# Kernel optimization log

Measured on AMD Instinct MI355X. Metric: run time of the kernel, lower is better.

Reference implementation:

```python
import jax, jax.numpy as jnp
import numpy as np

D = 16      # chem_dims
K = 16      # hard-coded k in Atom_embedding
N = 81920   # query points
M = 20000   # atoms
EPS = 1e-5  # BatchNorm eps


def _knn_idx(x, y, x_batch, y_batch, k, chunk=1024):
    """Block-diagonal kNN: indices of k nearest atoms in y for each point in x,
    restricted to matching batch ids (mirrors pykeops diagonal_ranges)."""
    n = x.shape[0]
    nch = n // chunk
    yb = y_batch[None, :]

    def f(args):
        xc, xbc = args                                            # [chunk,3], [chunk]
        d = jnp.sum((xc[:, None, :] - y[None, :, :]) ** 2, -1)    # [chunk, M]
        d = jnp.where(xbc[:, None] == yb, d, jnp.inf)
        _, idx = jax.lax.top_k(-d, k)                             # k smallest dists
        return idx

    idx = jax.lax.map(f, (x.reshape(nch, chunk, 3), x_batch.reshape(nch, chunk)))
    return idx.reshape(n, k)


def _bn_eval(h, gamma, beta, mean, var):
    # eval-mode BatchNorm1d over last dim
    return (h - mean) * (gamma * jax.lax.rsqrt(var + EPS)) + beta


def setup_inputs() -> dict:
    key = jax.random.key(0)
    ks = jax.random.split(key, 12)
    inp = {
        "x": jax.random.uniform(ks[0], (N, 3), jnp.float32) * 10.0,
        "y": jax.random.uniform(ks[1], (M, 3), jnp.float32) * 10.0,
        "y_atomtypes": jax.random.normal(ks[2], (M, D), jnp.float32),
        "x_batch": jnp.zeros((N,), jnp.int32),
        "y_batch": jnp.zeros((M,), jnp.int32),
        "W1": jax.random.normal(ks[3], (D + 1, D), jnp.float32) * 0.1,
        "b1": jnp.zeros((D,), jnp.float32),
        "W2": jax.random.normal(ks[4], (D, D), jnp.float32) * 0.1,
        "b2": jnp.zeros((D,), jnp.float32),
        "W3": jax.random.normal(ks[5], (2 * D, D), jnp.float32) * 0.1,
        "b3": jnp.zeros((D,), jnp.float32),
        "bn1_g": jnp.ones((D,), jnp.float32),
        "bn1_b": jnp.zeros((D,), jnp.float32),
        "bn1_m": jax.random.normal(ks[6], (D,), jnp.float32) * 0.1,
        "bn1_v": jnp.ones((D,), jnp.float32),
        "bn2_g": jnp.ones((D,), jnp.float32),
        "bn2_b": jnp.zeros((D,), jnp.float32),
        "bn2_m": jax.random.normal(ks[7], (D,), jnp.float32) * 0.1,
        "bn2_v": jnp.ones((D,), jnp.float32),
    }
    return inp


def reference(x, y, y_atomtypes, x_batch, y_batch,
              W1, b1, W2, b2, W3, b3,
              bn1_g, bn1_b, bn1_m, bn1_v,
              bn2_g, bn2_b, bn2_m, bn2_v):
    idx = _knn_idx(x, y, x_batch, y_batch, K)            # [N, K] int32
    yk = y[idx]                                          # [N, K, 3]
    dists = jnp.sum((x[:, None, :] - yk) ** 2, -1)       # [N, K]
    feat = jnp.concatenate(
        [y_atomtypes[idx], (1.0 / dists)[..., None]], -1)  # [N, K, D+1]
    # dropout in eval mode == identity
    h = feat @ W1 + b1                                   # conv1
    h = _bn_eval(jax.nn.leaky_relu(h, 0.2), bn1_g, bn1_b, bn1_m, bn1_v)
    fx1 = jnp.sum(h, axis=1)                             # [N, D]
    h2 = h @ W2 + b2                                     # conv2
    h2 = _bn_eval(jax.nn.leaky_relu(h2, 0.2), bn2_g, bn2_b, bn2_m, bn2_v)
    fx2 = jnp.sum(h2, axis=1)                            # [N, D]
    out = jnp.concatenate([fx1, fx2], -1) @ W3 + b3      # conv3 -> [N, D]
    return out
```

## Files before the change

kernel.cpp:

```cpp
#include <hip/hip_runtime.h>

#define N_PTS 81920
#define M_PTS 20000
#define NC 13
#define NCELLS 2197
#define CELLW 0.7692307692f
#define INVCELL 1.3f
#define BIGF 3.0e38f
#define CAP_STAGE 312
#define PPC 16
#define WPB 4
#define MAX_TASKS 7320

__device__ __forceinline__ int clampi(int v, int lo, int hi) {
  return v < lo ? lo : (v > hi ? hi : v);
}
__device__ __forceinline__ int cell_coord(float p) {
  return clampi((int)(p * INVCELL), 0, NC - 1);
}
__device__ __forceinline__ float floorpack(float d) {
  return __uint_as_float(__float_as_uint(d) & 0xFFFF8000u);
}


__global__ void hist_both_kernel(const float* __restrict__ y, const float* __restrict__ x,
                                 int* __restrict__ ycnt, int* __restrict__ xcnt) {
  int i = blockIdx.x * blockDim.x + threadIdx.x;
  if (i < M_PTS) {
    int c = (cell_coord(y[3*i+2])*NC + cell_coord(y[3*i+1]))*NC + cell_coord(y[3*i]);
    atomicAdd(&ycnt[c], 1);
  } else {
    int j = i - M_PTS;
    if (j < N_PTS) {
      int c = (cell_coord(x[3*j+2])*NC + cell_coord(x[3*j+1]))*NC + cell_coord(x[3*j]);
      atomicAdd(&xcnt[c], 1);
    }
  }
}

__global__ void scan2_kernel(const int* __restrict__ ycnt, int* __restrict__ ystart, int* __restrict__ ycur,
                             const int* __restrict__ xcnt, int* __restrict__ xstart, int* __restrict__ xcur) {
  const int* cnt = (blockIdx.x == 0) ? ycnt : xcnt;
  int* start     = (blockIdx.x == 0) ? ystart : xstart;
  int* cursor    = (blockIdx.x == 0) ? ycur : xcur;
  __shared__ int tmp[1024];
  int tid = threadIdx.x;
  int chunk = (NCELLS + 1023) >> 10;
  int base = tid * chunk;
  int sum = 0;
  for (int k = 0; k < chunk; ++k) {
    int j = base + k;
    if (j < NCELLS) sum += cnt[j];
  }
  tmp[tid] = sum;
  __syncthreads();
  for (int off = 1; off < 1024; off <<= 1) {
    int v = (tid >= off) ? tmp[tid - off] : 0;
    __syncthreads();
    tmp[tid] += v;
    __syncthreads();
  }
  int run = tmp[tid] - sum;
  for (int k = 0; k < chunk; ++k) {
    int j = base + k;
    if (j < NCELLS) { start[j] = run; cursor[j] = run; run += cnt[j]; }
  }
  if (tid == 1023) start[NCELLS] = tmp[1023];
}

__global__ void scatter_both_kernel(const float* __restrict__ y, const float* __restrict__ x,
                                    int* __restrict__ ycur, int* __restrict__ xcur,
                                    float4* __restrict__ ys4, int* __restrict__ xorder,
                                    float4* __restrict__ xs4) {
  int i = blockIdx.x * blockDim.x + threadIdx.x;
  if (i < M_PTS) {
    float px = y[3*i], py = y[3*i+1], pz = y[3*i+2];
    int c = (cell_coord(pz)*NC + cell_coord(py))*NC + cell_coord(px);
    int pos = atomicAdd(&ycur[c], 1);
    ys4[pos] = make_float4(px, py, pz, __int_as_float(i));
  } else {
    int j = i - M_PTS;
    if (j < N_PTS) {
      float px = x[3*j], py = x[3*j+1], pz = x[3*j+2];
      int c = (cell_coord(pz)*NC + cell_coord(py))*NC + cell_coord(px);
      int pos = atomicAdd(&xcur[c], 1);
      xorder[pos] = j;
      if (xs4) xs4[pos] = make_float4(px, py, pz, __int_as_float(j));
    }
  }
}

__global__ void build_tasks_kernel(const int* __restrict__ xstart,
                                   int* __restrict__ tasks, int* __restrict__ ntasks) {
  int c = blockIdx.x * blockDim.x + threadIdx.x;
  if (c >= NCELLS) return;
  int cnt = xstart[c+1] - xstart[c];
  int nch = (cnt + PPC - 1) / PPC;
  if (nch > 0) {
    int pos = atomicAdd(ntasks, nch);
    for (int k = 0; k < nch; ++k) tasks[pos + k] = (k << 12) | c;
  }
}

__global__ void sortcell_kernel(float4* __restrict__ ys4, const int* __restrict__ ystart) {
  int c = blockIdx.x * blockDim.x + threadIdx.x;
  if (c >= NCELLS) return;
  int r0 = ystart[c], r1 = ystart[c+1];
  for (int i = r0 + 1; i < r1; ++i) {
    float4 v = ys4[i];
    int key = __float_as_int(v.w);
    int j = i - 1;
    while (j >= r0 && __float_as_int(ys4[j].w) > key) { ys4[j+1] = ys4[j]; --j; }
    ys4[j+1] = v;
  }
}

__device__ __forceinline__ void bitonic_sort16(float (&d)[16]) {
  #define CE(a,b) { float lo=fminf(d[a],d[b]); float hi=fmaxf(d[a],d[b]); d[a]=lo; d[b]=hi; }
  CE(0,8) CE(1,9) CE(2,10) CE(3,11) CE(4,12) CE(5,13) CE(6,14) CE(7,15)
  CE(0,4) CE(1,5) CE(2,6) CE(3,7) CE(8,12) CE(9,13) CE(10,14) CE(11,15)
  CE(0,2) CE(1,3) CE(4,6) CE(5,7) CE(8,10) CE(9,11) CE(12,14) CE(13,15)
  CE(0,1) CE(2,3) CE(4,5) CE(6,7) CE(8,9) CE(10,11) CE(12,13) CE(14,15)
  #undef CE
}

__device__ __forceinline__ void ins16(float (&s)[16], float k) {
  #pragma unroll
  for (int j = 15; j >= 1; --j) s[j] = fminf(fmaxf(s[j-1], k), s[j]);
  s[0] = fminf(s[0], k);
}

__global__ void __launch_bounds__(256) knn_cell_kernel(
    const float4* __restrict__ xs4,
    const float4* __restrict__ ys4, const int* __restrict__ ystart,
    const int* __restrict__ xstart,
    const int* __restrict__ tasks, const int* __restrict__ ntasks,
    unsigned short* __restrict__ pi)
{
  __shared__ float4 cand_all[WPB][CAP_STAGE];
  int wid = threadIdx.x >> 6;
  int tid = threadIdx.x & 63;
  int ti = blockIdx.x * WPB + wid;
  if (ti >= ntasks[0]) return;
  int task = tasks[ti];
  int c = task & 4095, chunk = task >> 12;
  int cbeg = xstart[c];
  int cend = xstart[c+1];
  int pbeg = cbeg + chunk*PPC;
  int pend = min(cend, pbeg + PPC);

  float4* cand = cand_all[wid];

  int ccx = c % NC, ccy = (c / NC) % NC, ccz = c / (NC*NC);
  int x0 = ccx-1 < 0 ? 0 : ccx-1, x1 = ccx+1 > NC-1 ? NC-1 : ccx+1;
  int y0 = ccy-1 < 0 ? 0 : ccy-1, y1 = ccy+1 > NC-1 ? NC-1 : ccy+1;
  int z0 = ccz-1 < 0 ? 0 : ccz-1, z1 = ccz+1 > NC-1 ? NC-1 : ccz+1;

  int off = 0, nst = 0; bool ovf = false;
  for (int gz = z0; gz <= z1; ++gz) {
    for (int gy = y0; gy <= y1; ++gy) {
      int rowbase = (gz*NC + gy)*NC;
      int r0 = ystart[rowbase + x0];
      int r1 = ystart[rowbase + x1 + 1];
      int len = r1 - r0;
      if (!ovf && off + len <= CAP_STAGE) {
        for (int k = tid; k < len; k += 64) cand[off + k] = ys4[r0 + k];
        off += len; ++nst;
      } else ovf = true;
    }
  }
  int L = off;
  asm volatile("s_waitcnt vmcnt(0) lgkmcnt(0)" ::: "memory");

  int g = tid >> 2, sub = tid & 3;
  int pidx = pbeg + g;
  bool active = pidx < pend;
  int gid = active ? pidx : (pend - 1);
  float4 xq = xs4[gid];
  float xpx = xq.x, xpy = xq.y, xpz = xq.z;

  float s[16];
  #pragma unroll
  for (int j = 0; j < 16; ++j) s[j] = BIGF;

  auto packkey = [&](float4 q) -> float {
    float dx = xpx - q.x, dy = xpy - q.y, dz = xpz - q.z;
    float d = fmaf(dx, dx, fmaf(dy, dy, dz*dz));
    unsigned kb = (__float_as_uint(d) & 0xFFFF8000u) | (__float_as_uint(q.w) & 0x7FFFu);
    return __uint_as_float(kb);
  };

  auto merged16 = [&](float (&u)[16]) {
    float cb[16];
    #pragma unroll
    for (int i = 0; i < 16; ++i) cb[i] = fminf(s[i], __shfl_xor(s[15-i], 1));
    bitonic_sort16(cb);
    #pragma unroll
    for (int i = 0; i < 16; ++i) u[i] = fminf(cb[i], __shfl_xor(cb[15-i], 2));
    bitonic_sort16(u);
  };

  {
    int i = sub;
    for (; i + 4 < L; i += 8) {
      float4 q0 = cand[i], q1 = cand[i+4];
      float k0 = packkey(q0), k1 = packkey(q1);
      ins16(s, k0); ins16(s, k1);
    }
    for (; i < L; i += 4) ins16(s, packkey(cand[i]));
  }

  auto scan_row_g = [&](int xa, int xb, int rowbase) {
    int r0 = ystart[rowbase + xa];
    int r1 = ystart[rowbase + xb + 1];
    int i = r0 + sub;
    for (; i + 4 < r1; i += 8) {
      float4 q0 = ys4[i], q1 = ys4[i+4];
      float k0 = packkey(q0), k1 = packkey(q1);
      ins16(s, k0); ins16(s, k1);
    }
    for (; i < r1; i += 4) ins16(s, packkey(ys4[i]));
  };

  if (ovf) {
    int cnt2 = 0;
    for (int gz = z0; gz <= z1; ++gz)
      for (int gy = y0; gy <= y1; ++gy) {
        if (cnt2 >= nst) scan_row_g(x0, x1, (gz*NC + gy)*NC);
        ++cnt2;
      }
  }

  float u[16];
  merged16(u);
  float s15m = u[15];
  int R = 1;
  while (true) {
    float b = BIGF;
    if (ccx - R >= 0)    b = fminf(b, xpx - (float)(ccx-R)*CELLW);
    if (ccx + R <= NC-2) b = fminf(b, (float)(ccx+R+1)*CELLW - xpx);
    if (ccy - R >= 0)    b = fminf(b, xpy - (float)(ccy-R)*CELLW);
    if (ccy + R <= NC-2) b = fminf(b, (float)(ccy+R+1)*CELLW - xpy);
    if (ccz - R >= 0)    b = fminf(b, xpz - (float)(ccz-R)*CELLW);
    if (ccz + R <= NC-2) b = fminf(b, (float)(ccz+R+1)*CELLW - xpz);
    b = fmaxf(b - 1e-4f, 0.0f);
    if (s15m <= floorpack(b*b) || R >= NC) break;
    ++R;
    int z0r = ccz-R < 0 ? 0 : ccz-R, z1r = ccz+R > NC-1 ? NC-1 : ccz+R;
    int y0r = ccy-R < 0 ? 0 : ccy-R, y1r = ccy+R > NC-1 ? NC-1 : ccy+R;
    int x0r = ccx-R < 0 ? 0 : ccx-R, x1r = ccx+R > NC-1 ? NC-1 : ccx+R;
    for (int gz = z0r; gz <= z1r; ++gz) {
      int dzz = gz - ccz; if (dzz < 0) dzz = -dzz;
      float gapz = (gz > ccz) ? ((float)gz*CELLW - xpz)
                 : ((gz < ccz) ? (xpz - (float)(gz+1)*CELLW) : 0.0f);
      gapz = fmaxf(gapz - 1e-4f, 0.0f);
      float gz2 = gapz * gapz;
      for (int gy = y0r; gy <= y1r; ++gy) {
        int dyy = gy - ccy; if (dyy < 0) dyy = -dyy;
        float gapy = (gy > ccy) ? ((float)gy*CELLW - xpy)
                   : ((gy < ccy) ? (xpy - (float)(gy+1)*CELLW) : 0.0f);
        gapy = fmaxf(gapy - 1e-4f, 0.0f);
        float rowd2 = fmaf(gapy, gapy, gz2);
        if (floorpack(rowd2) >= s15m) continue;
        int rowbase = (gz*NC + gy)*NC;
        if (dzz == R || dyy == R) {
          scan_row_g(x0r, x1r, rowbase);
        } else {
          if (ccx - R >= 0) {
            float gapx = fmaxf(xpx - (float)(ccx-R+1)*CELLW - 1e-4f, 0.0f);
            if (floorpack(fmaf(gapx, gapx, rowd2)) < s15m)
              scan_row_g(ccx-R, ccx-R, rowbase);
          }
          if (ccx + R <= NC-1) {
            float gapx = fmaxf((float)(ccx+R)*CELLW - xpx - 1e-4f, 0.0f);
            if (floorpack(fmaf(gapx, gapx, rowd2)) < s15m)
              scan_row_g(ccx+R, ccx+R, rowbase);
          }
        }
      }
    }
    merged16(u);
    s15m = u[15];
  }

  if (active) {
    float v0 = u[sub*4+0], v1 = u[sub*4+1], v2 = u[sub*4+2], v3 = u[sub*4+3];
    unsigned wlo = (__float_as_uint(v0) & 0x7FFFu) | ((__float_as_uint(v1) & 0x7FFFu) << 16);
    unsigned whi = (__float_as_uint(v2) & 0x7FFFu) | ((__float_as_uint(v3) & 0x7FFFu) << 16);
    uint2 W; W.x = wlo; W.y = whi;
    ((uint2*)pi)[gid*4 + sub] = W;
  }
}

template<int CTRL>
__device__ __forceinline__ float ror_add(float v) {
  int r = __builtin_amdgcn_update_dpp(0, __float_as_int(v), CTRL, 0xF, 0xF, true);
  return v + __int_as_float(r);
}
__device__ __forceinline__ float red16(float v) {
  v = ror_add<0x121>(v);
  v = ror_add<0x122>(v);
  v = ror_add<0x124>(v);
  v = ror_add<0x128>(v);
  return v;
}

__global__ void __launch_bounds__(256) mlp_kernel(
    const float* __restrict__ yat, const float4* __restrict__ xs4, const float* __restrict__ y,
    const float* __restrict__ W1, const float* __restrict__ b1,
    const float* __restrict__ W2, const float* __restrict__ b2,
    const float* __restrict__ W3, const float* __restrict__ b3,
    const float* __restrict__ g1, const float* __restrict__ be1,
    const float* __restrict__ m1, const float* __restrict__ v1,
    const float* __restrict__ g2, const float* __restrict__ be2,
    const float* __restrict__ m2, const float* __restrict__ v2,
    const unsigned short* __restrict__ pi, float* __restrict__ out)
{
  int t = threadIdx.x;
  int o = t & 15;
  int gid = (blockIdx.x * 256 + t) >> 4;
  float4 xq = xs4[gid];
  int p = __float_as_int(xq.w);

  int id = (int)pi[gid*16 + o];
  float dx = xq.x - y[3*id], dy = xq.y - y[3*id+1], dz = xq.z - y[3*id+2];
  float dist = fmaf(dx, dx, fmaf(dy, dy, dz*dz));
  float invd = 1.0f / dist;

  const float4* a4 = (const float4*)(yat + ((size_t)id << 4));
  float4 q0 = a4[0], q1 = a4[1], q2 = a4[2], q3 = a4[3];
  float a[16];
  a[0]=q0.x; a[1]=q0.y; a[2]=q0.z; a[3]=q0.w;
  a[4]=q1.x; a[5]=q1.y; a[6]=q1.z; a[7]=q1.w;
  a[8]=q2.x; a[9]=q2.y; a[10]=q2.z; a[11]=q2.w;
  a[12]=q3.x; a[13]=q3.y; a[14]=q3.z; a[15]=q3.w;

  float h[16];
  #pragma unroll
  for (int oo = 0; oo < 16; ++oo) {
    float acc = fmaf(invd, W1[256 + oo], b1[oo]);
    #pragma unroll
    for (int i = 0; i < 16; ++i) acc = fmaf(a[i], W1[i*16 + oo], acc);
    acc = fmaxf(acc, 0.2f * acc);
    float S = g1[oo] * rsqrtf(v1[oo] + 1e-5f);
    h[oo] = fmaf(acc - m1[oo], S, be1[oo]);
  }

  float f2[16];
  #pragma unroll
  for (int oo = 0; oo < 16; ++oo) {
    float acc = b2[oo];
    #pragma unroll
    for (int i = 0; i < 16; ++i) acc = fmaf(h[i], W2[i*16 + oo], acc);
    acc = fmaxf(acc, 0.2f * acc);
    float S = g2[oo] * rsqrtf(v2[oo] + 1e-5f);
    f2[oo] = fmaf(acc - m2[oo], S, be2[oo]);
  }

  float acc = b3[o];
  #pragma unroll
  for (int i = 0; i < 16; ++i) acc = fmaf(red16(h[i]),  W3[i*16 + o], acc);
  #pragma unroll
  for (int i = 0; i < 16; ++i) acc = fmaf(red16(f2[i]), W3[(16 + i)*16 + o], acc);

  out[(size_t)p*16 + o] = acc;
}

__device__ __forceinline__ void stage_weights(float* lds, int t,
    const float* W1, const float* b1, const float* W2, const float* b2,
    const float* W3, const float* b3,
    const float* g1, const float* be1, const float* m1, const float* v1,
    const float* g2, const float* be2, const float* m2, const float* v2)
{
  for (int k = t; k < 272; k += 256) { int i = k >> 4, o = k & 15; lds[o*20 + i] = W1[k]; }
  for (int k = t; k < 256; k += 256) { int i = k >> 4, o = k & 15; lds[320 + o*16 + i] = W2[k]; }
  for (int k = t; k < 512; k += 256) { int i = k >> 4, o = k & 15; lds[576 + o*32 + i] = W3[k]; }
  if (t < 16) {
    lds[1088 + t] = b1[t];
    lds[1104 + t] = b2[t];
    lds[1120 + t] = b3[t];
    float s1 = g1[t] * rsqrtf(v1[t] + 1e-5f);
    lds[1136 + t] = s1;
    lds[1152 + t] = be1[t] - m1[t]*s1;
    float s2 = g2[t] * rsqrtf(v2[t] + 1e-5f);
    lds[1168 + t] = s2;
    lds[1184 + t] = be2[t] - m2[t]*s2;
  }
}

__device__ __forceinline__ void topk_insert(float (&s)[16], int (&si)[16], float d, int qi) {
  #pragma unroll
  for (int j = 15; j >= 1; --j) {
    bool c1 = d < s[j-1];
    bool c2 = d < s[j];
    float ns = c1 ? s[j-1] : (c2 ? d : s[j]);
    int  ni = c1 ? si[j-1] : (c2 ? qi : si[j]);
    s[j] = ns; si[j] = ni;
  }
  if (d < s[0]) { si[0] = qi; s[0] = d; }
}

__device__ __forceinline__ void mlp_and_store(const float* lds, const float2* spill, int t,
    const float* __restrict__ yat, float* __restrict__ out, int p)
{
  const float* W1t = lds;
  const float* W2t = lds + 320;
  const float* W3t = lds + 576;
  const float* sb1 = lds + 1088;
  const float* sb2 = lds + 1104;
  const float* sb3 = lds + 1120;
  const float* S1 = lds + 1136;
  const float* T1 = lds + 1152;
  const float* S2 = lds + 1168;
  const float* T2 = lds + 1184;

  float fx1[16], fx2[16];
  #pragma unroll
  for (int o = 0; o < 16; ++o) { fx1[o] = 0.0f; fx2[o] = 0.0f; }

  #pragma unroll 1
  for (int j = 0; j < 16; ++j) {
    float2 sv = spill[j*256 + t];
    float invd = 1.0f / sv.x;
    int id = __float_as_int(sv.y);
    const float4* a4 = (const float4*)(yat + ((size_t)id << 4));
    float4 q0 = a4[0], q1 = a4[1], q2 = a4[2], q3 = a4[3];
    float a[16];
    a[0]=q0.x; a[1]=q0.y; a[2]=q0.z; a[3]=q0.w;
    a[4]=q1.x; a[5]=q1.y; a[6]=q1.z; a[7]=q1.w;
    a[8]=q2.x; a[9]=q2.y; a[10]=q2.z; a[11]=q2.w;
    a[12]=q3.x; a[13]=q3.y; a[14]=q3.z; a[15]=q3.w;
    float h[16];
    #pragma unroll
    for (int o = 0; o < 16; ++o) {
      float acc = fmaf(invd, W1t[o*20 + 16], sb1[o]);
      #pragma unroll
      for (int i = 0; i < 16; ++i) acc = fmaf(a[i], W1t[o*20 + i], acc);
      acc = fmaxf(acc, 0.2f * acc);
      float hv = fmaf(acc, S1[o], T1[o]);
      h[o] = hv;
      fx1[o] += hv;
    }
    #pragma unroll
    for (int o = 0; o < 16; ++o) {
      float acc = sb2[o];
      #pragma unroll
      for (int i = 0; i < 16; ++i) acc = fmaf(h[i], W2t[o*16 + i], acc);
      acc = fmaxf(acc, 0.2f * acc);
      fx2[o] += fmaf(acc, S2[o], T2[o]);
    }
  }

  float res[16];
  #pragma unroll
  for (int o = 0; o < 16; ++o) {
    float acc = sb3[o];
    #pragma unroll
    for (int i = 0; i < 16; ++i) acc = fmaf(fx1[i], W3t[o*32 + i], acc);
    #pragma unroll
    for (int i = 0; i < 16; ++i) acc = fmaf(fx2[i], W3t[o*32 + 16 + i], acc);
    res[o] = acc;
  }
  float* op = out + ((size_t)p << 4);
  float4 r;
  r.x=res[0]; r.y=res[1]; r.z=res[2]; r.w=res[3];   ((float4*)op)[0] = r;
  r.x=res[4]; r.y=res[5]; r.z=res[6]; r.w=res[7];   ((float4*)op)[1] = r;
  r.x=res[8]; r.y=res[9]; r.z=res[10]; r.w=res[11]; ((float4*)op)[2] = r;
  r.x=res[12]; r.y=res[13]; r.z=res[14]; r.w=res[15];((float4*)op)[3] = r;
}

__global__ void __launch_bounds__(256) knn_mlp_fused_kernel(
    const float* __restrict__ x, const float* __restrict__ yat,
    const float* __restrict__ W1, const float* __restrict__ b1,
    const float* __restrict__ W2, const float* __restrict__ b2,
    const float* __restrict__ W3, const float* __restrict__ b3,
    const float* __restrict__ g1, const float* __restrict__ be1,
    const float* __restrict__ m1, const float* __restrict__ v1,
    const float* __restrict__ g2, const float* __restrict__ be2,
    const float* __restrict__ m2, const float* __restrict__ v2,
    const float4* __restrict__ ys4, const int* __restrict__ ystart,
    const int* __restrict__ xorder, float* __restrict__ out)
{
  __shared__ float lds[1200];
  __shared__ float2 spill[4096];
  int t = threadIdx.x;
  stage_weights(lds, t, W1,b1,W2,b2,W3,b3, g1,be1,m1,v1, g2,be2,m2,v2);
  __syncthreads();

  int gid = blockIdx.x * 256 + t;
  int p = xorder[gid];
  float xpx = x[3*p], xpy = x[3*p+1], xpz = x[3*p+2];
  int cx = cell_coord(xpx), cy = cell_coord(xpy), cz = cell_coord(xpz);

  float s[16]; int si[16];
  #pragma unroll
  for (int j = 0; j < 16; ++j) { s[j] = BIGF; si[j] = 0; }

  auto scan_row = [&](int gz, int gy, int xa, int xb) {
    int rowbase = (gz*NC + gy)*NC;
    int r0 = ystart[rowbase + xa];
    int r1 = ystart[rowbase + xb + 1];
    for (int i = r0; i < r1; ++i) {
      float4 q = ys4[i];
      float dx = xpx - q.x, dy = xpy - q.y, dz = xpz - q.z;
      float d = fmaf(dx, dx, fmaf(dy, dy, dz*dz));
      if (d < s[15]) topk_insert(s, si, d, __float_as_int(q.w));
    }
  };

  {
    int z0 = cz-1 < 0 ? 0 : cz-1, z1 = cz+1 > NC-1 ? NC-1 : cz+1;
    int y0 = cy-1 < 0 ? 0 : cy-1, y1 = cy+1 > NC-1 ? NC-1 : cy+1;
    int x0 = cx-1 < 0 ? 0 : cx-1, x1 = cx+1 > NC-1 ? NC-1 : cx+1;
    for (int gz = z0; gz <= z1; ++gz)
      for (int gy = y0; gy <= y1; ++gy)
        scan_row(gz, gy, x0, x1);
  }

  int R = 1;
  while (true) {
    float b = BIGF;
    if (cx - R >= 0)    b = fminf(b, xpx - (float)(cx-R)*CELLW);
    if (cx + R <= NC-2) b = fminf(b, (float)(cx+R+1)*CELLW - xpx);
    if (cy - R >= 0)    b = fminf(b, xpy - (float)(cy-R)*CELLW);
    if (cy + R <= NC-2) b = fminf(b, (float)(cy+R+1)*CELLW - xpy);
    if (cz - R >= 0)    b = fminf(b, xpz - (float)(cz-R)*CELLW);
    if (cz + R <= NC-2) b = fminf(b, (float)(cz+R+1)*CELLW - xpz);
    b = fmaxf(b - 1e-4f, 0.0f);
    if (s[15] <= b*b || R >= NC) break;
    ++R;
    int z0 = cz-R < 0 ? 0 : cz-R, z1 = cz+R > NC-1 ? NC-1 : cz+R;
    int y0 = cy-R < 0 ? 0 : cy-R, y1 = cy+R > NC-1 ? NC-1 : cy+R;
    int x0 = cx-R < 0 ? 0 : cx-R, x1 = cx+R > NC-1 ? NC-1 : cx+R;
    for (int gz = z0; gz <= z1; ++gz) {
      int dzz = gz - cz; if (dzz < 0) dzz = -dzz;
      for (int gy = y0; gy <= y1; ++gy) {
        int dyy = gy - cy; if (dyy < 0) dyy = -dyy;
        if (dzz == R || dyy == R) {
          scan_row(gz, gy, x0, x1);
        } else {
          if (cx - R >= 0)    scan_row(gz, gy, cx-R, cx-R);
          if (cx + R <= NC-1) scan_row(gz, gy, cx+R, cx+R);
        }
      }
    }
  }

  #pragma unroll
  for (int j = 0; j < 16; ++j) spill[j*256 + t] = make_float2(s[j], __int_as_float(si[j]));
  mlp_and_store(lds, spill, t, yat, out, p);
}

__global__ void __launch_bounds__(256) brute_kernel(
    const float* __restrict__ x, const float* __restrict__ y, const float* __restrict__ yat,
    const float* __restrict__ W1, const float* __restrict__ b1,
    const float* __restrict__ W2, const float* __restrict__ b2,
    const float* __restrict__ W3, const float* __restrict__ b3,
    const float* __restrict__ g1, const float* __restrict__ be1,
    const float* __restrict__ m1, const float* __restrict__ v1,
    const float* __restrict__ g2, const float* __restrict__ be2,
    const float* __restrict__ m2, const float* __restrict__ v2,
    float* __restrict__ out)
{
  __shared__ float lds[1200];
  __shared__ float2 spill[4096];
  __shared__ float4 ybuf[1024];
  int t = threadIdx.x;
  stage_weights(lds, t, W1,b1,W2,b2,W3,b3, g1,be1,m1,v1, g2,be2,m2,v2);

  int gid = blockIdx.x * 256 + t;
  float xpx = x[3*gid], xpy = x[3*gid+1], xpz = x[3*gid+2];
  float s[16]; int si[16];
  #pragma unroll
  for (int j = 0; j < 16; ++j) { s[j] = BIGF; si[j] = 0; }

  for (int base = 0; base < M_PTS; base += 1024) {
    int nload = M_PTS - base; if (nload > 1024) nload = 1024;
    __syncthreads();
    for (int k = t; k < nload; k += 256) {
      int i = base + k;
      ybuf[k] = make_float4(y[3*i], y[3*i+1], y[3*i+2], __int_as_float(i));
    }
    __syncthreads();
    for (int i2 = 0; i2 < nload; ++i2) {
      float4 q = ybuf[i2];
      float dx = xpx - q.x, dy = xpy - q.y, dz = xpz - q.z;
      float d = fmaf(dx, dx, fmaf(dy, dy, dz*dz));
      if (d < s[15]) topk_insert(s, si, d, __float_as_int(q.w));
    }
  }

  #pragma unroll
  for (int j = 0; j < 16; ++j) spill[j*256 + t] = make_float2(s[j], __int_as_float(si[j]));
  mlp_and_store(lds, spill, t, yat, out, gid);
}

extern "C" void kernel_launch(void* const* d_in, const int* in_sizes, int n_in,
                              void* d_out, int out_size, void* d_ws, size_t ws_size,
                              hipStream_t stream) {
  const float* x   = (const float*)d_in[0];
  const float* y   = (const float*)d_in[1];
  const float* yat = (const float*)d_in[2];
  const float* W1  = (const float*)d_in[5];
  const float* b1  = (const float*)d_in[6];
  const float* W2  = (const float*)d_in[7];
  const float* b2  = (const float*)d_in[8];
  const float* W3  = (const float*)d_in[9];
  const float* b3  = (const float*)d_in[10];
  const float* g1  = (const float*)d_in[11];
  const float* be1 = (const float*)d_in[12];
  const float* m1  = (const float*)d_in[13];
  const float* v1  = (const float*)d_in[14];
  const float* g2  = (const float*)d_in[15];
  const float* be2 = (const float*)d_in[16];
  const float* m2  = (const float*)d_in[17];
  const float* v2  = (const float*)d_in[18];
  float* out = (float*)d_out;

  const size_t WS_SPLIT = 4661936;
  const size_t WS_FUSED = 700480;

  if (ws_size >= WS_SPLIT) {
    char* ws = (char*)d_ws;
    float4* ys4 = (float4*)(ws);
    float4* xs4 = (float4*)(ws + 320000);
    int* xorder = (int*)(ws + 1630720);
    unsigned short* pi = (unsigned short*)(ws + 1958400);
    int* ycnt   = (int*)(ws + 4579840);
    int* xcnt   = (int*)(ws + 4588640);
    int* ystart = (int*)(ws + 4597440);
    int* ycur   = (int*)(ws + 4606240);
    int* xstart = (int*)(ws + 4615040);
    int* xcur   = (int*)(ws + 4623840);
    int* ntasks = (int*)(ws + 4632640);
    int* tasks  = (int*)(ws + 4632656);

    hipMemsetAsync(ws + 4579840, 0, 17600, stream);
    hipMemsetAsync(ws + 4632640, 0, 16, stream);
    int grid_mn = (M_PTS + N_PTS + 255) / 256;
    hist_both_kernel<<<grid_mn, 256, 0, stream>>>(y, x, ycnt, xcnt);
    scan2_kernel<<<2, 1024, 0, stream>>>(ycnt, ystart, ycur, xcnt, xstart, xcur);
    scatter_both_kernel<<<grid_mn, 256, 0, stream>>>(y, x, ycur, xcur, ys4, xorder, xs4);
    build_tasks_kernel<<<(NCELLS+255)/256, 256, 0, stream>>>(xstart, tasks, ntasks);
    knn_cell_kernel<<<MAX_TASKS/WPB, 256, 0, stream>>>(xs4, ys4, ystart, xstart,
        tasks, ntasks, pi);
    mlp_kernel<<<(N_PTS*16)/256, 256, 0, stream>>>(yat, xs4, y, W1,b1,W2,b2,W3,b3,
        g1,be1,m1,v1, g2,be2,m2,v2, pi, out);
  } else if (ws_size >= WS_FUSED) {
    char* ws = (char*)d_ws;
    float4* ys4 = (float4*)(ws);
    int* xorder = (int*)(ws + 320000);
    int* ycnt   = (int*)(ws + 647680);
    int* xcnt   = (int*)(ws + 656480);
    int* ystart = (int*)(ws + 665280);
    int* ycur   = (int*)(ws + 674080);
    int* xstart = (int*)(ws + 682880);
    int* xcur   = (int*)(ws + 691680);

    hipMemsetAsync(ws + 647680, 0, 17588, stream);
    int grid_mn = (M_PTS + N_PTS + 255) / 256;
    hist_both_kernel<<<grid_mn, 256, 0, stream>>>(y, x, ycnt, xcnt);
    scan2_kernel<<<2, 1024, 0, stream>>>(ycnt, ystart, ycur, xcnt, xstart, xcur);
    scatter_both_kernel<<<grid_mn, 256, 0, stream>>>(y, x, ycur, xcur, ys4, xorder, nullptr);
    sortcell_kernel<<<(NCELLS+255)/256, 256, 0, stream>>>(ys4, ystart);
    knn_mlp_fused_kernel<<<N_PTS/256, 256, 0, stream>>>(x, yat, W1,b1,W2,b2,W3,b3,
        g1,be1,m1,v1, g2,be2,m2,v2, ys4, ystart, xorder, out);
  } else {
    brute_kernel<<<N_PTS/256, 256, 0, stream>>>(x, y, yat, W1,b1,W2,b2,W3,b3,
        g1,be1,m1,v1, g2,be2,m2,v2, out);
  }
}
```

Before: 122.3 us.

## Refine grid to 14^3 cells, fold task building into scan, pad atom coords

The spatial grid goes from 13^3 to 14^3 cells, so each cell holds fewer atoms and kNN candidate scanning shrinks, with the staging capacity and max task count adjusted to match. Task-list construction moves into the second block of the scan kernel as a deterministic prefix sum, which removes the separate build_tasks launch and its atomics along with one memset. The scatter kernel also writes a float4-padded copy of the atom coordinates so the MLP kernel can load each neighbor's position in one vector read instead of three scalar reads. The costs are a larger workspace requirement, a serial per-thread task write loop in the scan, and a smaller staging capacity that could overflow for dense cells.

```diff
diff --git a/kernel.cpp b/kernel.cpp
--- a/kernel.cpp
+++ b/kernel.cpp
@@ -2,15 +2,15 @@
 
 #define N_PTS 81920
 #define M_PTS 20000
-#define NC 13
-#define NCELLS 2197
-#define CELLW 0.7692307692f
-#define INVCELL 1.3f
+#define NC 14
+#define NCELLS 2744
+#define CELLW 0.7142857143f
+#define INVCELL 1.4f
 #define BIGF 3.0e38f
-#define CAP_STAGE 312
+#define CAP_STAGE 264
 #define PPC 16
 #define WPB 4
-#define MAX_TASKS 7320
+#define MAX_TASKS 7880
 
 __device__ __forceinline__ int clampi(int v, int lo, int hi) {
   return v < lo ? lo : (v > hi ? hi : v);
@@ -39,7 +39,8 @@
 }
 
 __global__ void scan2_kernel(const int* __restrict__ ycnt, int* __restrict__ ystart, int* __restrict__ ycur,
-                             const int* __restrict__ xcnt, int* __restrict__ xstart, int* __restrict__ xcur) {
+                             const int* __restrict__ xcnt, int* __restrict__ xstart, int* __restrict__ xcur,
+                             int* __restrict__ tasks, int* __restrict__ ntasks) {
   const int* cnt = (blockIdx.x == 0) ? ycnt : xcnt;
   int* start     = (blockIdx.x == 0) ? ystart : xstart;
   int* cursor    = (blockIdx.x == 0) ? ycur : xcur;
@@ -66,15 +67,42 @@
     if (j < NCELLS) { start[j] = run; cursor[j] = run; run += cnt[j]; }
   }
   if (tid == 1023) start[NCELLS] = tmp[1023];
+
+  if (blockIdx.x == 1) {
+    int tsum = 0;
+    for (int k = 0; k < chunk; ++k) {
+      int j = base + k;
+      if (j < NCELLS) tsum += (cnt[j] + PPC - 1) / PPC;
+    }
+    __syncthreads();
+    tmp[tid] = tsum;
+    __syncthreads();
+    for (int off = 1; off < 1024; off <<= 1) {
+      int v = (tid >= off) ? tmp[tid - off] : 0;
+      __syncthreads();
+      tmp[tid] += v;
+      __syncthreads();
+    }
+    int trun = tmp[tid] - tsum;
+    for (int k = 0; k < chunk; ++k) {
+      int j = base + k;
+      if (j < NCELLS) {
+        int nch = (cnt[j] + PPC - 1) / PPC;
+        for (int q2 = 0; q2 < nch; ++q2) tasks[trun++] = (q2 << 12) | j;
+      }
+    }
+    if (tid == 1023) ntasks[0] = tmp[1023];
+  }
 }
 
 __global__ void scatter_both_kernel(const float* __restrict__ y, const float* __restrict__ x,
                                     int* __restrict__ ycur, int* __restrict__ xcur,
                                     float4* __restrict__ ys4, int* __restrict__ xorder,
-                                    float4* __restrict__ xs4) {
+                                    float4* __restrict__ xs4, float4* __restrict__ y4) {
   int i = blockIdx.x * blockDim.x + threadIdx.x;
   if (i < M_PTS) {
     float px = y[3*i], py = y[3*i+1], pz = y[3*i+2];
+    if (y4) y4[i] = make_float4(px, py, pz, 0.0f);
     int c = (cell_coord(pz)*NC + cell_coord(py))*NC + cell_coord(px);
     int pos = atomicAdd(&ycur[c], 1);
     ys4[pos] = make_float4(px, py, pz, __int_as_float(i));
@@ -87,18 +115,6 @@
       xorder[pos] = j;
       if (xs4) xs4[pos] = make_float4(px, py, pz, __int_as_float(j));
     }
-  }
-}
-
-__global__ void build_tasks_kernel(const int* __restrict__ xstart,
-                                   int* __restrict__ tasks, int* __restrict__ ntasks) {
-  int c = blockIdx.x * blockDim.x + threadIdx.x;
-  if (c >= NCELLS) return;
-  int cnt = xstart[c+1] - xstart[c];
-  int nch = (cnt + PPC - 1) / PPC;
-  if (nch > 0) {
-    int pos = atomicAdd(ntasks, nch);
-    for (int k = 0; k < nch; ++k) tasks[pos + k] = (k << 12) | c;
   }
 }
 
@@ -306,7 +322,7 @@
 }
 
 __global__ void __launch_bounds__(256) mlp_kernel(
-    const float* __restrict__ yat, const float4* __restrict__ xs4, const float* __restrict__ y,
+    const float* __restrict__ yat, const float4* __restrict__ xs4, const float4* __restrict__ y4,
     const float* __restrict__ W1, const float* __restrict__ b1,
     const float* __restrict__ W2, const float* __restrict__ b2,
     const float* __restrict__ W3, const float* __restrict__ b3,
@@ -323,7 +339,8 @@
   int p = __float_as_int(xq.w);
 
   int id = (int)pi[gid*16 + o];
-  float dx = xq.x - y[3*id], dy = xq.y - y[3*id+1], dz = xq.z - y[3*id+2];
+  float4 yq = y4[id];
+  float dx = xq.x - yq.x, dy = xq.y - yq.y, dz = xq.z - yq.z;
   float dist = fmaf(dx, dx, fmaf(dy, dy, dz*dz));
   float invd = 1.0f / dist;
 
@@ -617,51 +634,54 @@
   const float* v2  = (const float*)d_in[18];
   float* out = (float*)d_out;
 
-  const size_t WS_SPLIT = 4661936;
-  const size_t WS_FUSED = 700480;
+  const size_t WS_SPLIT = 4997424;
+  const size_t WS_FUSED = 760000;
 
   if (ws_size >= WS_SPLIT) {
     char* ws = (char*)d_ws;
     float4* ys4 = (float4*)(ws);
-    float4* xs4 = (float4*)(ws + 320000);
-    int* xorder = (int*)(ws + 1630720);
-    unsigned short* pi = (unsigned short*)(ws + 1958400);
-    int* ycnt   = (int*)(ws + 4579840);
-    int* xcnt   = (int*)(ws + 4588640);
-    int* ystart = (int*)(ws + 4597440);
-    int* ycur   = (int*)(ws + 4606240);
-    int* xstart = (int*)(ws + 4615040);
-    int* xcur   = (int*)(ws + 4623840);
-    int* ntasks = (int*)(ws + 4632640);
-    int* tasks  = (int*)(ws + 4632656);
-
-    hipMemsetAsync(ws + 4579840, 0, 17600, stream);
-    hipMemsetAsync(ws + 4632640, 0, 16, stream);
+    float4* y4  = (float4*)(ws + 320000);
+    float4* xs4 = (float4*)(ws + 640000);
+    int* xorder = (int*)(ws + 1950720);
+    unsigned short* pi = (unsigned short*)(ws + 2278400);
+    int* ycnt   = (int*)(ws + 4899840);
+    int* xcnt   = (int*)(ws + 4910848);
+    int* ystart = (int*)(ws + 4921856);
+    int* ycur   = (int*)(ws + 4932864);
+    int* xstart = (int*)(ws + 4943872);
+    int* xcur   = (int*)(ws + 4954880);
+    int* ntasks = (int*)(ws + 4965888);
+    int* tasks  = (int*)(ws + 4965904);
+
+    hipMemsetAsync(ws + 4899840, 0, 22016, stream);
     int grid_mn = (M_PTS + N_PTS + 255) / 256;
     hist_both_kernel<<<grid_mn, 256, 0, stream>>>(y, x, ycnt, xcnt);
-    scan2_kernel<<<2, 1024, 0, stream>>>(ycnt, ystart, ycur, xcnt, xstart, xcur);
-    scatter_both_kernel<<<grid_mn, 256, 0, stream>>>(y, x, ycur, xcur, ys4, xorder, xs4);
-    build_tasks_kernel<<<(NCELLS+255)/256, 256, 0, stream>>>(xstart, tasks, ntasks);
+    scan2_kernel<<<2, 1024, 0, stream>>>(ycnt, ystart, ycur, xcnt, xstart, xcur,
+                                         tasks, ntasks);
+    scatter_both_kernel<<<grid_mn, 256, 0, stream>>>(y, x, ycur, xcur, ys4, xorder, xs4, y4);
     knn_cell_kernel<<<MAX_TASKS/WPB, 256, 0, stream>>>(xs4, ys4, ystart, xstart,
         tasks, ntasks, pi);
-    mlp_kernel<<<(N_PTS*16)/256, 256, 0, stream>>>(yat, xs4, y, W1,b1,W2,b2,W3,b3,
+    mlp_kernel<<<(N_PTS*16)/256, 256, 0, stream>>>(yat, xs4, y4, W1,b1,W2,b2,W3,b3,
         g1,be1,m1,v1, g2,be2,m2,v2, pi, out);
   } else if (ws_size >= WS_FUSED) {
     char* ws = (char*)d_ws;
     float4* ys4 = (float4*)(ws);
     int* xorder = (int*)(ws + 320000);
     int* ycnt   = (int*)(ws + 647680);
-    int* xcnt   = (int*)(ws + 656480);
-    int* ystart = (int*)(ws + 665280);
-    int* ycur   = (int*)(ws + 674080);
-    int* xstart = (int*)(ws + 682880);
-    int* xcur   = (int*)(ws + 691680);
-
-    hipMemsetAsync(ws + 647680, 0, 17588, stream);
+    int* xcnt   = (int*)(ws + 658688);
+    int* ystart = (int*)(ws + 669696);
+    int* ycur   = (int*)(ws + 680704);
+    int* xstart = (int*)(ws + 691712);
+    int* xcur   = (int*)(ws + 702720);
+    int* tasks  = (int*)(ws + 713728);
+    int* ntasks = (int*)(ws + 713728);
+
+    hipMemsetAsync(ws + 647680, 0, 22016, stream);
     int grid_mn = (M_PTS + N_PTS + 255) / 256;
     hist_both_kernel<<<grid_mn, 256, 0, stream>>>(y, x, ycnt, xcnt);
-    scan2_kernel<<<2, 1024, 0, stream>>>(ycnt, ystart, ycur, xcnt, xstart, xcur);
-    scatter_both_kernel<<<grid_mn, 256, 0, stream>>>(y, x, ycur, xcur, ys4, xorder, nullptr);
+    scan2_kernel<<<2, 1024, 0, stream>>>(ycnt, ystart, ycur, xcnt, xstart, xcur,
+                                         tasks + 4, ntasks);
+    scatter_both_kernel<<<grid_mn, 256, 0, stream>>>(y, x, ycur, xcur, ys4, xorder, nullptr, nullptr);
     sortcell_kernel<<<(NCELLS+255)/256, 256, 0, stream>>>(ys4, ystart);
     knn_mlp_fused_kernel<<<N_PTS/256, 256, 0, stream>>>(x, yat, W1,b1,W2,b2,W3,b3,
         g1,be1,m1,v1, g2,be2,m2,v2, ys4, ystart, xorder, out);
```

Measured after the change: 115.3 us (median of 3 runs). 5.7% less time.
